# Performance work log

Measured on AMD Instinct MI355X. Metric: run time of the kernel, lower is better.

The kernel has to match this reference:

```python
import jax, jax.numpy as jnp
import numpy as np

BN_EPS = 1e-5


def setup_inputs() -> dict:
    key = jax.random.key(0)
    ks = jax.random.split(key, 10)
    B, C, Ci, H, W = 4, 256, 128, 64, 64
    s = 0.05
    return {
        "x": jax.random.normal(ks[0], (B, C, H, W), jnp.float32),
        "g_w": jax.random.normal(ks[1], (Ci, C), jnp.float32) * s,
        "g_b": jax.random.normal(ks[2], (Ci,), jnp.float32) * s,
        "theta_w": jax.random.normal(ks[3], (Ci, C), jnp.float32) * s,
        "theta_b": jax.random.normal(ks[4], (Ci,), jnp.float32) * s,
        "phi_w": jax.random.normal(ks[5], (Ci, C), jnp.float32) * s,
        "phi_b": jax.random.normal(ks[6], (Ci,), jnp.float32) * s,
        "W_w": jax.random.normal(ks[7], (C, Ci), jnp.float32) * s,
        "W_b": jax.random.normal(ks[8], (C,), jnp.float32) * s,
        "bn_gamma": jnp.ones((C,), jnp.float32),
        "bn_beta": jnp.zeros((C,), jnp.float32),
        "scale": jax.random.normal(ks[9], (1,), jnp.float32),
    }


def reference(x, g_w, g_b, theta_w, theta_b, phi_w, phi_b, W_w, W_b, bn_gamma, bn_beta, scale):
    B, C, H, W = x.shape
    xf = x.reshape(B, C, H * W)  # [B, C, N]
    # 1x1 conv projections == channel matmuls
    g = jnp.einsum('oc,bcn->bno', g_w, xf) + g_b            # [B, N, Ci]
    th = jnp.einsum('oc,bcn->bno', theta_w, xf) + theta_b   # [B, N, Ci]
    ph = jnp.einsum('oc,bcn->bon', phi_w, xf) + phi_b[:, None]  # [B, Ci, N]
    # unscaled attention: f = theta @ phi, softmax over keys
    f = jnp.einsum('bnd,bdm->bnm', th, ph)                  # [B, N, N]
    attn = jax.nn.softmax(f, axis=-1)
    y = jnp.einsum('bnm,bmo->bno', attn, g)                 # [B, N, Ci]
    y4 = y.transpose(0, 2, 1).reshape(B, -1, H, W)          # [B, Ci, H, W]
    # W: 1x1 conv + BatchNorm2d (training mode: batch statistics)
    wy = jnp.einsum('od,bdhw->bohw', W_w, y4) + W_b[None, :, None, None]
    mean = wy.mean(axis=(0, 2, 3))
    var = wy.var(axis=(0, 2, 3))
    bn = (wy - mean[None, :, None, None]) * jax.lax.rsqrt(var[None, :, None, None] + BN_EPS)
    bn = bn * bn_gamma[None, :, None, None] + bn_beta[None, :, None, None]
    return scale * bn + x
```

## Files before the change

kernel.cpp:

```cpp
#include <hip/hip_runtime.h>
#include <hip/hip_bf16.h>

#define BB 4
#define CC 256
#define CI 128
#define NN 4096

typedef _Float16 f16;
typedef __attribute__((ext_vector_type(8))) _Float16 f16x8;
typedef __attribute__((ext_vector_type(4))) _Float16 f16x4;
typedef __attribute__((ext_vector_type(4))) float f32x4;

#define MFMA(a,b,c) __builtin_amdgcn_mfma_f32_16x16x32_f16(a,b,c,0,0,0)
#define LDS3(p) ((__attribute__((address_space(3))) void*)(p))
#define GL1(p)  ((const __attribute__((address_space(1))) void*)(p))

__global__ __launch_bounds__(256) void k01_xpose(const float* x, f16* xt,
                                                 const float* tw, const float* pw,
                                                 const float* gw, const float* Ww, f16* wdst){
    int nt = blockIdx.x, ct = blockIdx.y, b = blockIdx.z;
    __shared__ float tile[64][65];
    int t = threadIdx.x;
    const float* src = x + ((size_t)(b*CC + ct*64))*NN + nt*64;
    #pragma unroll
    for (int k=0;k<16;k++){ int idx=t+k*256; int cl=idx>>6, nl=idx&63;
        tile[cl][nl]=src[(size_t)cl*NN + nl]; }
    __syncthreads();
    f16* dst = xt + ((size_t)(b*NN + nt*64))*CC + ct*64;
    #pragma unroll
    for (int k=0;k<16;k++){ int idx=t+k*256; int nl=idx>>6, cl=idx&63;
        dst[(size_t)nl*CC + cl] = (f16)tile[cl][nl]; }
    if (t < 128){
        int blkId = blockIdx.x + 64*(blockIdx.y + 4*blockIdx.z);
        int i = blkId*128 + t;
        int j = i & 32767; int sel = i >> 15;
        const float* s = (sel==0)? tw : (sel==1)? pw : (sel==2)? gw : Ww;
        wdst[i] = (f16)s[j];
    }
}

__global__ __launch_bounds__(256) void k2_all(const f16* xt, const f16* thw, const f16* phw,
                                              const f16* gwh, const float* thb, const float* phb,
                                              const float* gb, f16* th, f16* ph, f16* gt2){
    int b = blockIdx.y; int xx = blockIdx.x;
    int wv = threadIdx.x>>6, lane = threadIdx.x&63, q=lane>>4, cc=lane&15;
    if (xx < 64){
        int mat = xx>>5; int ntile = xx&31;
        int n0 = ntile*128 + wv*32;
        f16x8 aq[2][8];
        #pragma unroll
        for (int ns=0;ns<2;ns++){
            const f16* ap = xt + ((size_t)(b*NN + n0 + ns*16 + cc))*CC + q*8;
            #pragma unroll
            for (int kk=0;kk<8;kk++) aq[ns][kk] = *(const f16x8*)(ap + kk*32);
        }
        const f16* w   = mat? phw : thw;
        const float* bias = mat? phb : thb;
        f16* o = mat? ph : th;
        #pragma unroll 2
        for (int os=0;os<8;os++){
            f32x4 acc0={0,0,0,0}, acc1={0,0,0,0};
            const f16* wp = w + ((size_t)(os*16 + cc))*CC + q*8;
            #pragma unroll
            for (int kk=0;kk<8;kk++){
                f16x8 bf = *(const f16x8*)(wp + kk*32);
                acc0 = MFMA(aq[0][kk], bf, acc0);
                acc1 = MFMA(aq[1][kk], bf, acc1);
            }
            float bv = bias[os*16+cc];
            #pragma unroll
            for (int r=0;r<4;r++){
                o[((size_t)(b*NN + n0      + 4*q + r))*CI + os*16 + cc] = (f16)(acc0[r] + bv);
                o[((size_t)(b*NN + n0 + 16 + 4*q + r))*CI + os*16 + cc] = (f16)(acc1[r] + bv);
            }
        }
    } else {
        int mt = xx - 64;
        f16x8 ag[2][8];
        #pragma unroll
        for (int os=0;os<2;os++){
            const f16* ap = gwh + ((size_t)(wv*32 + os*16 + cc))*CC + q*8;
            #pragma unroll
            for (int kk=0;kk<8;kk++) ag[os][kk] = *(const f16x8*)(ap + kk*32);
        }
        f32x4 acc[2][4];
        #pragma unroll
        for (int os=0;os<2;os++){
            #pragma unroll
            for (int ms=0;ms<4;ms++) acc[os][ms]=(f32x4){0,0,0,0};
        }
        #pragma unroll 2
        for (int kk=0;kk<8;kk++){
            #pragma unroll
            for (int ms=0;ms<4;ms++){
                f16x8 bf = *(const f16x8*)(xt + ((size_t)(b*NN + mt*64 + ms*16 + cc))*CC + kk*32 + q*8);
                acc[0][ms]=MFMA(ag[0][kk],bf,acc[0][ms]);
                acc[1][ms]=MFMA(ag[1][kk],bf,acc[1][ms]);
            }
        }
        #pragma unroll
        for (int os=0;os<2;os++){
            #pragma unroll
            for (int r=0;r<4;r++){
                int orow = wv*32 + os*16 + 4*q + r;
                float bv = gb[orow];
                #pragma unroll
                for (int ms=0;ms<4;ms++){
                    int pos = (ms>>1)*32 + 8*(cc>>2) + 4*(ms&1) + (cc&3);
                    gt2[((size_t)(b*64 + mt))*8192 + orow*64 + pos] = (f16)(acc[os][ms][r] + bv);
                }
            }
        }
    }
}

__global__ __launch_bounds__(256, 2) void k3_attn(const f16* th, const f16* ph, const f16* gt2,
                                                  f16* ypart, float* ml){
    int qt = blockIdx.x;
    int sp = blockIdx.y;
    int b  = blockIdx.z;
    int wv=threadIdx.x>>6, lane=threadIdx.x&63, q=lane>>4, cc=lane&15;
    int qrow0 = qt*128 + wv*32;
    int kv0 = sp*1024;
    int sw  = cc<<4;
    int rsw = (cc&7)<<4;

    __shared__ __align__(16) char ldsb[65536];
    char* phL = ldsb;
    char* gtL = ldsb + 32768;

    f16x8 aq[2][4];
    #pragma unroll
    for (int rb=0;rb<2;rb++){
        const f16* thp = th + ((size_t)(b*NN + qrow0 + rb*16 + cc))*CI + q*8;
        #pragma unroll
        for (int kk=0;kk<4;kk++) aq[rb][kk] = *(const f16x8*)(thp + kk*32);
    }

    const char* phg = (const char*)(ph + (size_t)b*NN*CI);
    const char* gtg = (const char*)gt2 + (size_t)b*64*16384;

    f32x4 yacc[2][8];
    #pragma unroll
    for (int rb=0;rb<2;rb++)
        #pragma unroll
        for (int os=0;os<8;os++) yacc[rb][os]=(f32x4){0,0,0,0};
    float m_run0=-1e30f, m_run1=-1e30f, l_run0=0.f, l_run1=0.f;

    auto STAGE = [&](int tt, int bb){
        int key0 = kv0 + tt*64;
        int mt  = key0 >> 6;
        char* pbase = phL + bb*16384 + wv*4096;
        char* gbase = gtL + bb*16384 + wv*4096;
        #pragma unroll
        for (int ch=0; ch<4; ch++){
            int prow = wv*16 + ch*4 + (lane>>4);
            const char* ps = phg + (size_t)(key0 + prow)*256 + (((lane&15)*16) ^ ((prow&15)<<4));
            __builtin_amdgcn_global_load_lds(GL1(ps), LDS3(pbase + ch*1024), 16, 0, 0);
            int gf = wv*4096 + ch*1024 + lane*16;
            int grow = gf>>7, gcol = gf&127;
            int scol = gcol ^ ((grow&7)<<4);
            const char* gs = gtg + (size_t)mt*16384 + grow*128 + scol;
            __builtin_amdgcn_global_load_lds(GL1(gs), LDS3(gbase + ch*1024), 16, 0, 0);
        }
    };

    STAGE(0, 0);
    __syncthreads();

    int cur = 0;
    #pragma unroll 1
    for (int it=0; it<16; ++it){
        if (it < 15) STAGE(it+1, cur^1);
        const char* pt  = phL + cur*16384;
        const char* gtt = gtL + cur*16384;
        f32x4 fa[2][4];
        #pragma unroll
        for (int j=0;j<4;j++){
            f16x8 pf[4];
            #pragma unroll
            for (int kk=0;kk<4;kk++)
                pf[kk] = *(const f16x8*)(pt + (j*16+cc)*256 + ((kk*64 + q*16) ^ sw));
            fa[0][j]=(f32x4){0,0,0,0}; fa[1][j]=(f32x4){0,0,0,0};
            #pragma unroll
            for (int kk=0;kk<4;kk++){
                fa[0][j]=MFMA(pf[kk], aq[0][kk], fa[0][j]);
                fa[1][j]=MFMA(pf[kk], aq[1][kk], fa[1][j]);
            }
        }
        float pm0 = fmaxf(fmaxf(fmaxf(fa[0][0][0],fa[0][0][1]),fmaxf(fa[0][0][2],fa[0][0][3])),
                          fmaxf(fmaxf(fa[0][1][0],fa[0][1][1]),fmaxf(fa[0][1][2],fa[0][1][3])));
        pm0 = fmaxf(pm0, fmaxf(fmaxf(fa[0][2][0],fa[0][2][1]),fmaxf(fa[0][2][2],fa[0][2][3])));
        pm0 = fmaxf(pm0, fmaxf(fmaxf(fa[0][3][0],fa[0][3][1]),fmaxf(fa[0][3][2],fa[0][3][3])));
        float pm1 = fmaxf(fmaxf(fmaxf(fa[1][0][0],fa[1][0][1]),fmaxf(fa[1][0][2],fa[1][0][3])),
                          fmaxf(fmaxf(fa[1][1][0],fa[1][1][1]),fmaxf(fa[1][1][2],fa[1][1][3])));
        pm1 = fmaxf(pm1, fmaxf(fmaxf(fa[1][2][0],fa[1][2][1]),fmaxf(fa[1][2][2],fa[1][2][3])));
        pm1 = fmaxf(pm1, fmaxf(fmaxf(fa[1][3][0],fa[1][3][1]),fmaxf(fa[1][3][2],fa[1][3][3])));
        if (__any(fmaxf(pm0 - m_run0, pm1 - m_run1) > 3.f)){
            float mx0 = pm0;
            mx0 = fmaxf(mx0, __shfl_xor(mx0,16));
            mx0 = fmaxf(mx0, __shfl_xor(mx0,32));
            float mx1 = pm1;
            mx1 = fmaxf(mx1, __shfl_xor(mx1,16));
            mx1 = fmaxf(mx1, __shfl_xor(mx1,32));
            float nm0 = fmaxf(m_run0, mx0), nm1 = fmaxf(m_run1, mx1);
            float co0 = __expf(m_run0 - nm0), co1 = __expf(m_run1 - nm1);
            m_run0 = nm0; m_run1 = nm1;
            l_run0 *= co0; l_run1 *= co1;
            #pragma unroll
            for (int os=0;os<8;os++){ yacc[0][os] *= co0; yacc[1][os] *= co1; }
        }
        #pragma unroll
        for (int j=0;j<4;j++){
            #pragma unroll
            for (int r=0;r<4;r++){
                fa[0][j][r] = __expf(fa[0][j][r]-m_run0);
                fa[1][j][r] = __expf(fa[1][j][r]-m_run1);
            }
        }
        l_run0 += ((fa[0][0][0]+fa[0][0][1]+fa[0][0][2]+fa[0][0][3])
                 + (fa[0][1][0]+fa[0][1][1]+fa[0][1][2]+fa[0][1][3]))
                + ((fa[0][2][0]+fa[0][2][1]+fa[0][2][2]+fa[0][2][3])
                 + (fa[0][3][0]+fa[0][3][1]+fa[0][3][2]+fa[0][3][3]));
        l_run1 += ((fa[1][0][0]+fa[1][0][1]+fa[1][0][2]+fa[1][0][3])
                 + (fa[1][1][0]+fa[1][1][1]+fa[1][1][2]+fa[1][1][3]))
                + ((fa[1][2][0]+fa[1][2][1]+fa[1][2][2]+fa[1][2][3])
                 + (fa[1][3][0]+fa[1][3][1]+fa[1][3][2]+fa[1][3][3]));
        f16x8 pb0h0, pb0h1, pb1h0, pb1h1;
        #pragma unroll
        for (int r=0;r<4;r++){
            pb0h0[r]=(f16)fa[0][0][r]; pb0h0[4+r]=(f16)fa[0][1][r];
            pb0h1[r]=(f16)fa[0][2][r]; pb0h1[4+r]=(f16)fa[0][3][r];
            pb1h0[r]=(f16)fa[1][0][r]; pb1h0[4+r]=(f16)fa[1][1][r];
            pb1h1[r]=(f16)fa[1][2][r]; pb1h1[4+r]=(f16)fa[1][3][r];
        }
        #pragma unroll
        for (int os=0;os<8;os++){
            int row = os*16 + cc;
            f16x8 ga0 = *(const f16x8*)(gtt + row*128 + (((0<<6)|(q<<4)) ^ rsw));
            f16x8 ga1 = *(const f16x8*)(gtt + row*128 + (((1<<6)|(q<<4)) ^ rsw));
            yacc[0][os] = MFMA(ga0, pb0h0, yacc[0][os]);
            yacc[1][os] = MFMA(ga0, pb1h0, yacc[1][os]);
            yacc[0][os] = MFMA(ga1, pb0h1, yacc[0][os]);
            yacc[1][os] = MFMA(ga1, pb1h1, yacc[1][os]);
        }
        __syncthreads();
        cur ^= 1;
    }
    float l0 = l_run0; l0 += __shfl_xor(l0,16); l0 += __shfl_xor(l0,32);
    float l1 = l_run1; l1 += __shfl_xor(l1,16); l1 += __shfl_xor(l1,32);
    float linv0 = 1.f/l0, linv1 = 1.f/l1;
    f16* yl = (f16*)(ldsb + wv*8192);
    #pragma unroll
    for (int os=0;os<8;os++){
        #pragma unroll
        for (int r=0;r<4;r++){
            int o = os*16 + 4*q + r;
            *(f16*)((char*)yl + cc*256      + ((o*2) ^ ((cc&7)<<4))) = (f16)(yacc[0][os][r]*linv0);
            *(f16*)((char*)yl + (16+cc)*256 + ((o*2) ^ ((cc&7)<<4))) = (f16)(yacc[1][os][r]*linv1);
        }
    }
    #pragma unroll
    for (int p=0;p<8;p++){
        int idx = p*512 + lane*8;
        int row = idx>>7, o0 = idx&127;
        f16x8 v = *(const f16x8*)((char*)yl + row*256 + ((o0*2) ^ ((row&7)<<4)));
        *(f16x8*)(ypart + ((size_t)((sp*4+b)*NN + qrow0 + row))*CI + o0) = v;
    }
    if (lane < 16){
        size_t row0 = (size_t)(sp*4+b)*NN + qrow0 + lane;
        ml[row0*2]        = m_run0;
        ml[row0*2+1]      = l0;
        ml[(row0+16)*2]   = m_run1;
        ml[(row0+16)*2+1] = l1;
    }
}

__global__ __launch_bounds__(256) void k3c(const f16* ypart, const float* ml,
                                           f16* y, float* part, float* mupart){
    int blk = blockIdx.x; int t = threadIdx.x;
    int rloc = t>>2;
    int row  = blk*64 + rloc;
    int b = row>>12, n = row & 4095;
    int o0 = (t&3)*32;
    __shared__ __align__(16) f16 ldsT[128*64];
    float m_s[4], l_s[4];
    #pragma unroll
    for (int s=0;s<4;s++){ size_t r2 = ((size_t)(s*4+b)*NN + n)*2; m_s[s]=ml[r2]; l_s[s]=ml[r2+1]; }
    float M = fmaxf(fmaxf(m_s[0],m_s[1]),fmaxf(m_s[2],m_s[3]));
    float w[4]; float L=0.f;
    #pragma unroll
    for (int s=0;s<4;s++){ w[s]=l_s[s]*__expf(m_s[s]-M); L+=w[s]; }
    float inv = 1.f/L;
    #pragma unroll
    for (int s=0;s<4;s++) w[s]*=inv;
    float acc[32];
    #pragma unroll
    for (int j=0;j<32;j++) acc[j]=0.f;
    #pragma unroll
    for (int s=0;s<4;s++){
        const f16* src = ypart + ((size_t)(s*4+b)*NN + n)*CI + o0;
        #pragma unroll
        for (int v=0;v<4;v++){
            f16x8 vv = *(const f16x8*)(src + v*8);
            #pragma unroll
            for (int e=0;e<8;e++) acc[v*8+e] += w[s]*(float)vv[e];
        }
    }
    f16* yo = y + (size_t)row*CI + o0;
    #pragma unroll
    for (int v=0;v<4;v++){
        f16x8 ov;
        #pragma unroll
        for (int e=0;e<8;e++) ov[e] = (f16)acc[v*8+e];
        *(f16x8*)(yo + v*8) = ov;
        #pragma unroll
        for (int e=0;e<8;e++){
            int o = o0 + v*8 + e;
            ldsT[o*64 + (rloc ^ ((o&7)<<3))] = ov[e];
        }
    }
    __syncthreads();
    int wv=t>>6, lane=t&63, q=lane>>4, cc=lane&15;
    f32x4 gacc[2][8];
    #pragma unroll
    for (int a=0;a<2;a++)
        #pragma unroll
        for (int c2=0;c2<8;c2++) gacc[a][c2]=(f32x4){0,0,0,0};
    f16x8 af[2][2];
    #pragma unroll
    for (int o1t=0;o1t<2;o1t++){
        int o1 = (wv*2+o1t)*16+cc;
        #pragma unroll
        for (int kk=0;kk<2;kk++)
            af[o1t][kk] = *(const f16x8*)(ldsT + o1*64 + ((kk*32+q*8) ^ ((o1&7)<<3)));
    }
    #pragma unroll 1
    for (int o2t=0;o2t<8;o2t++){
        int o2 = o2t*16+cc;
        #pragma unroll
        for (int kk=0;kk<2;kk++){
            f16x8 bf = *(const f16x8*)(ldsT + o2*64 + ((kk*32+q*8) ^ ((o2&7)<<3)));
            gacc[0][o2t] = MFMA(af[0][kk], bf, gacc[0][o2t]);
            gacc[1][o2t] = MFMA(af[1][kk], bf, gacc[1][o2t]);
        }
    }
    float* pb = part + (size_t)blk*16384;
    #pragma unroll
    for (int o1t=0;o1t<2;o1t++){
        #pragma unroll
        for (int o2t=0;o2t<8;o2t++){
            #pragma unroll
            for (int r=0;r<4;r++)
                pb[((wv*2+o1t)*16+4*q+r)*128 + o2t*16+cc] = gacc[o1t][o2t][r];
        }
    }
    if (t<128){
        float sm=0.f;
        #pragma unroll
        for (int v=0;v<8;v++){
            f16x8 vv = *(const f16x8*)(ldsT + t*64 + ((v*8) ^ ((t&7)<<3)));
            #pragma unroll
            for (int e=0;e<8;e++) sm += (float)vv[e];
        }
        mupart[blk*128 + t] = sm;
    }
}

__global__ __launch_bounds__(256) void k4b_red(const float* part, const float* mupart, float* S){
    int pc = blockIdx.y;
    int t = threadIdx.x;
    if (blockIdx.x < 64){
        int i = blockIdx.x*256 + t;
        float s=0.f;
        #pragma unroll 1
        for (int p=pc*32; p<pc*32+32; p++) s += part[(size_t)p*16384 + i];
        atomicAdd(&S[i], s);
    } else if (t < 128){
        float s=0.f;
        #pragma unroll 1
        for (int p=pc*32; p<pc*32+32; p++) s += mupart[p*128 + t];
        atomicAdd(&S[16384+t], s);
    }
}

__global__ __launch_bounds__(128) void k4c_coef(const float* S, const float* Ww, const float* Wb,
                                                const float* gamma, const float* beta,
                                                const float* scale, float* AB){
    int ch = blockIdx.x; int t = threadIdx.x;
    const float* w = Ww + ch*CI;
    float tmp=0.f;
    const float* Srow = S + t*CI;
    #pragma unroll 1
    for (int o2=0;o2<CI;o2++) tmp += Srow[o2]*w[o2];
    float v  = w[t]*tmp;
    float mc = w[t]*S[16384 + t];
    #pragma unroll
    for (int s=1;s<64;s<<=1){ v += __shfl_xor(v,s); mc += __shfl_xor(mc,s); }
    __shared__ float red[4];
    if ((t&63)==0){ red[(t>>6)*2]=v; red[(t>>6)*2+1]=mc; }
    __syncthreads();
    if (t==0){
        float wSw = red[0]+red[2];
        float wmu = red[1]+red[3];
        const float M = 16384.f;
        float meanwy = wmu/M + Wb[ch];
        float var = wSw/M - (wmu/M)*(wmu/M);
        float inv = rsqrtf(var + 1e-5f);
        float sc = scale[0];
        float A  = sc*gamma[ch]*inv;
        float B3 = sc*(beta[ch] - meanwy*inv*gamma[ch]);
        AB[ch]     = A;
        AB[256+ch] = B3 + A*Wb[ch];
    }
}

__global__ __launch_bounds__(256) void k5_out(const f16* Wwh, const f16* y, const float* x,
                                              const float* AB, float* out){
    int ntile = blockIdx.x;
    int cht   = blockIdx.y;
    int b     = blockIdx.z;
    int wv=threadIdx.x>>6, lane=threadIdx.x&63, q=lane>>4, cc=lane&15;
    int ch0 = cht*64 + wv*16;
    f16x8 aw[4];
    const f16* wp = Wwh + ((size_t)(ch0+cc))*CI + q*8;
    #pragma unroll
    for (int kk=0;kk<4;kk++) aw[kk]=*(const f16x8*)(wp+kk*32);
    float Ar[4], Br[4];
    #pragma unroll
    for (int r=0;r<4;r++){ Ar[r]=AB[ch0+4*q+r]; Br[r]=AB[256+ch0+4*q+r]; }
    #pragma unroll 2
    for (int ns=0;ns<8;ns++){
        int n0 = ntile*128 + ns*16;
        f32x4 acc={0,0,0,0};
        const f16* yp = y + ((size_t)(b*NN + n0 + cc))*CI + q*8;
        #pragma unroll
        for (int kk=0;kk<4;kk++) acc = MFMA(aw[kk], *(const f16x8*)(yp+kk*32), acc);
        #pragma unroll
        for (int r=0;r<4;r++){
            size_t addr = ((size_t)(b*CC + ch0 + 4*q + r))*NN + n0 + cc;
            out[addr] = x[addr] + Ar[r]*acc[r] + Br[r];
        }
    }
}

extern "C" void kernel_launch(void* const* d_in, const int* in_sizes, int n_in,
                              void* d_out, int out_size, void* d_ws, size_t ws_size,
                              hipStream_t stream){
    const float* x    = (const float*)d_in[0];
    const float* g_w  = (const float*)d_in[1];
    const float* g_b  = (const float*)d_in[2];
    const float* th_w = (const float*)d_in[3];
    const float* th_b = (const float*)d_in[4];
    const float* ph_w = (const float*)d_in[5];
    const float* ph_b = (const float*)d_in[6];
    const float* W_w  = (const float*)d_in[7];
    const float* W_b  = (const float*)d_in[8];
    const float* bg   = (const float*)d_in[9];
    const float* bb   = (const float*)d_in[10];
    const float* sc   = (const float*)d_in[11];

    char* ws = (char*)d_ws;
    f16* xt  = (f16*)(ws);
    f16* th  = (f16*)(ws + 8388608);
    f16* ph  = (f16*)(ws + 8388608 + 1*4194304);
    f16* gt2 = (f16*)(ws + 8388608 + 2*4194304);
    f16* y   = (f16*)(ws + 8388608 + 3*4194304);
    f16* wh  = (f16*)(ws + 8388608 + 4*4194304);
    float* ml    = (float*)(ws + 25427968);
    f16*   ypart = (f16*)(ws + 25952256);
    float* mupart= (float*)(ws + 42729472);
    float* part  = (float*)ws;
    float* S    = (float*)(ws + 42860544);
    float* AB   = (float*)(ws + 42926592);
    f16* th_wh = wh;
    f16* ph_wh = wh + 32768;
    f16* g_wh  = wh + 65536;
    f16* Ww_h  = wh + 98304;

    hipMemsetAsync(S, 0, 16512*sizeof(float), stream);
    hipLaunchKernelGGL(k01_xpose, dim3(64,4,4), dim3(256), 0, stream, x, xt, th_w, ph_w, g_w, W_w, wh);
    hipLaunchKernelGGL(k2_all,   dim3(128,4),   dim3(256), 0, stream, xt, th_wh, ph_wh, g_wh,
                       th_b, ph_b, g_b, th, ph, gt2);
    hipLaunchKernelGGL(k3_attn,  dim3(32,4,4),  dim3(256), 0, stream, th, ph, gt2, ypart, ml);
    hipLaunchKernelGGL(k3c,      dim3(256),     dim3(256), 0, stream, ypart, ml, y, part, mupart);
    hipLaunchKernelGGL(k4b_red,  dim3(65,8),    dim3(256), 0, stream, part, mupart, S);
    hipLaunchKernelGGL(k4c_coef, dim3(256),     dim3(128), 0, stream, S, W_w, W_b, bg, bb, sc, AB);
    hipLaunchKernelGGL(k5_out,   dim3(32,4,4),  dim3(256), 0, stream, Ww_h, y, x, AB, (float*)d_out);
}
```

Before: 138.6 us.

## Add 8-way key-split attention kernel with single-buffered phi and smaller LDS

Adds k3_attn8, which splits the key dimension into 8 chunks of 512 instead of 4 of 1024, doubling the grid to 1024 blocks. It single-buffers the phi tile in LDS (48KB total) and targets 3 blocks per CU, to raise occupancy and parallelism on the attention stage. The combine kernel now loops over a runtime split count, which doubles the partial-output traffic it reads and writes. The 8-way path is only used when the workspace is at least about 60MB, so whether it runs depends on the harness allocation.

After: 149.0 us. +7.5%, slower.

```diff
diff --git a/kernel.cpp b/kernel.cpp
--- a/kernel.cpp
+++ b/kernel.cpp
@@ -116,9 +116,7 @@
 
 __global__ __launch_bounds__(256, 2) void k3_attn(const f16* th, const f16* ph, const f16* gt2,
                                                   f16* ypart, float* ml){
-    int qt = blockIdx.x;
-    int sp = blockIdx.y;
-    int b  = blockIdx.z;
+    int qt = blockIdx.x; int sp = blockIdx.y; int b = blockIdx.z;
     int wv=threadIdx.x>>6, lane=threadIdx.x&63, q=lane>>4, cc=lane&15;
     int qrow0 = qt*128 + wv*32;
     int kv0 = sp*1024;
@@ -136,7 +134,6 @@
         #pragma unroll
         for (int kk=0;kk<4;kk++) aq[rb][kk] = *(const f16x8*)(thp + kk*32);
     }
-
     const char* phg = (const char*)(ph + (size_t)b*NN*CI);
     const char* gtg = (const char*)gt2 + (size_t)b*64*16384;
 
@@ -167,7 +164,6 @@
 
     STAGE(0, 0);
     __syncthreads();
-
     int cur = 0;
     #pragma unroll 1
     for (int it=0; it<16; ++it){
@@ -276,35 +272,208 @@
     }
 }
 
+__global__ __launch_bounds__(256, 3) void k3_attn8(const f16* th, const f16* ph, const f16* gt2,
+                                                   f16* ypart, float* ml){
+    int qt = blockIdx.x;
+    int sp = blockIdx.y;
+    int b  = blockIdx.z;
+    int wv=threadIdx.x>>6, lane=threadIdx.x&63, q=lane>>4, cc=lane&15;
+    int qrow0 = qt*128 + wv*32;
+    int kv0 = sp*512;
+    int sw  = cc<<4;
+    int rsw = (cc&7)<<4;
+
+    __shared__ __align__(16) char ldsb[49152];
+    char* phL = ldsb;
+    char* gtL = ldsb + 16384;
+
+    f16x8 aq[2][4];
+    #pragma unroll
+    for (int rb=0;rb<2;rb++){
+        const f16* thp = th + ((size_t)(b*NN + qrow0 + rb*16 + cc))*CI + q*8;
+        #pragma unroll
+        for (int kk=0;kk<4;kk++) aq[rb][kk] = *(const f16x8*)(thp + kk*32);
+    }
+    const char* phg = (const char*)(ph + (size_t)b*NN*CI);
+    const char* gtg = (const char*)gt2 + (size_t)b*64*16384;
+
+    f32x4 yacc[2][8];
+    #pragma unroll
+    for (int rb=0;rb<2;rb++)
+        #pragma unroll
+        for (int os=0;os<8;os++) yacc[rb][os]=(f32x4){0,0,0,0};
+    float m_run0=-1e30f, m_run1=-1e30f, l_run0=0.f, l_run1=0.f;
+
+    auto STAGE_PH = [&](int tt){
+        int key0 = kv0 + tt*64;
+        char* pbase = phL + wv*4096;
+        #pragma unroll
+        for (int ch=0; ch<4; ch++){
+            int prow = wv*16 + ch*4 + (lane>>4);
+            const char* ps = phg + (size_t)(key0 + prow)*256 + (((lane&15)*16) ^ ((prow&15)<<4));
+            __builtin_amdgcn_global_load_lds(GL1(ps), LDS3(pbase + ch*1024), 16, 0, 0);
+        }
+    };
+    auto STAGE_GT = [&](int tt, int bb){
+        int key0 = kv0 + tt*64;
+        int mt  = key0 >> 6;
+        char* gbase = gtL + bb*16384 + wv*4096;
+        #pragma unroll
+        for (int ch=0; ch<4; ch++){
+            int gf = wv*4096 + ch*1024 + lane*16;
+            int grow = gf>>7, gcol = gf&127;
+            int scol = gcol ^ ((grow&7)<<4);
+            const char* gs = gtg + (size_t)mt*16384 + grow*128 + scol;
+            __builtin_amdgcn_global_load_lds(GL1(gs), LDS3(gbase + ch*1024), 16, 0, 0);
+        }
+    };
+
+    STAGE_PH(0);
+    STAGE_GT(0, 0);
+    __syncthreads();
+
+    int cur = 0;
+    #pragma unroll 1
+    for (int it=0; it<8; ++it){
+        f32x4 fa[2][4];
+        #pragma unroll
+        for (int j=0;j<4;j++){
+            f16x8 pf[4];
+            #pragma unroll
+            for (int kk=0;kk<4;kk++)
+                pf[kk] = *(const f16x8*)(phL + (j*16+cc)*256 + ((kk*64 + q*16) ^ sw));
+            fa[0][j]=(f32x4){0,0,0,0}; fa[1][j]=(f32x4){0,0,0,0};
+            #pragma unroll
+            for (int kk=0;kk<4;kk++){
+                fa[0][j]=MFMA(pf[kk], aq[0][kk], fa[0][j]);
+                fa[1][j]=MFMA(pf[kk], aq[1][kk], fa[1][j]);
+            }
+        }
+        __syncthreads();
+        if (it < 7){
+            STAGE_PH(it+1);
+            STAGE_GT(it+1, cur^1);
+        }
+        float pm0 = fmaxf(fmaxf(fmaxf(fa[0][0][0],fa[0][0][1]),fmaxf(fa[0][0][2],fa[0][0][3])),
+                          fmaxf(fmaxf(fa[0][1][0],fa[0][1][1]),fmaxf(fa[0][1][2],fa[0][1][3])));
+        pm0 = fmaxf(pm0, fmaxf(fmaxf(fa[0][2][0],fa[0][2][1]),fmaxf(fa[0][2][2],fa[0][2][3])));
+        pm0 = fmaxf(pm0, fmaxf(fmaxf(fa[0][3][0],fa[0][3][1]),fmaxf(fa[0][3][2],fa[0][3][3])));
+        float pm1 = fmaxf(fmaxf(fmaxf(fa[1][0][0],fa[1][0][1]),fmaxf(fa[1][0][2],fa[1][0][3])),
+                          fmaxf(fmaxf(fa[1][1][0],fa[1][1][1]),fmaxf(fa[1][1][2],fa[1][1][3])));
+        pm1 = fmaxf(pm1, fmaxf(fmaxf(fa[1][2][0],fa[1][2][1]),fmaxf(fa[1][2][2],fa[1][2][3])));
+        pm1 = fmaxf(pm1, fmaxf(fmaxf(fa[1][3][0],fa[1][3][1]),fmaxf(fa[1][3][2],fa[1][3][3])));
+        if (__any(fmaxf(pm0 - m_run0, pm1 - m_run1) > 3.f)){
+            float mx0 = pm0;
+            mx0 = fmaxf(mx0, __shfl_xor(mx0,16));
+            mx0 = fmaxf(mx0, __shfl_xor(mx0,32));
+            float mx1 = pm1;
+            mx1 = fmaxf(mx1, __shfl_xor(mx1,16));
+            mx1 = fmaxf(mx1, __shfl_xor(mx1,32));
+            float nm0 = fmaxf(m_run0, mx0), nm1 = fmaxf(m_run1, mx1);
+            float co0 = __expf(m_run0 - nm0), co1 = __expf(m_run1 - nm1);
+            m_run0 = nm0; m_run1 = nm1;
+            l_run0 *= co0; l_run1 *= co1;
+            #pragma unroll
+            for (int os=0;os<8;os++){ yacc[0][os] *= co0; yacc[1][os] *= co1; }
+        }
+        #pragma unroll
+        for (int j=0;j<4;j++){
+            #pragma unroll
+            for (int r=0;r<4;r++){
+                fa[0][j][r] = __expf(fa[0][j][r]-m_run0);
+                fa[1][j][r] = __expf(fa[1][j][r]-m_run1);
+            }
+        }
+        l_run0 += ((fa[0][0][0]+fa[0][0][1]+fa[0][0][2]+fa[0][0][3])
+                 + (fa[0][1][0]+fa[0][1][1]+fa[0][1][2]+fa[0][1][3]))
+                + ((fa[0][2][0]+fa[0][2][1]+fa[0][2][2]+fa[0][2][3])
+                 + (fa[0][3][0]+fa[0][3][1]+fa[0][3][2]+fa[0][3][3]));
+        l_run1 += ((fa[1][0][0]+fa[1][0][1]+fa[1][0][2]+fa[1][0][3])
+                 + (fa[1][1][0]+fa[1][1][1]+fa[1][1][2]+fa[1][1][3]))
+                + ((fa[1][2][0]+fa[1][2][1]+fa[1][2][2]+fa[1][2][3])
+                 + (fa[1][3][0]+fa[1][3][1]+fa[1][3][2]+fa[1][3][3]));
+        f16x8 pb0h0, pb0h1, pb1h0, pb1h1;
+        #pragma unroll
+        for (int r=0;r<4;r++){
+            pb0h0[r]=(f16)fa[0][0][r]; pb0h0[4+r]=(f16)fa[0][1][r];
+            pb0h1[r]=(f16)fa[0][2][r]; pb0h1[4+r]=(f16)fa[0][3][r];
+            pb1h0[r]=(f16)fa[1][0][r]; pb1h0[4+r]=(f16)fa[1][1][r];
+            pb1h1[r]=(f16)fa[1][2][r]; pb1h1[4+r]=(f16)fa[1][3][r];
+        }
+        const char* gtt = gtL + cur*16384;
+        #pragma unroll
+        for (int os=0;os<8;os++){
+            int row = os*16 + cc;
+            f16x8 ga0 = *(const f16x8*)(gtt + row*128 + (((0<<6)|(q<<4)) ^ rsw));
+            f16x8 ga1 = *(const f16x8*)(gtt + row*128 + (((1<<6)|(q<<4)) ^ rsw));
+            yacc[0][os] = MFMA(ga0, pb0h0, yacc[0][os]);
+            yacc[1][os] = MFMA(ga0, pb1h0, yacc[1][os]);
+            yacc[0][os] = MFMA(ga1, pb0h1, yacc[0][os]);
+            yacc[1][os] = MFMA(ga1, pb1h1, yacc[1][os]);
+        }
+        __syncthreads();
+        cur ^= 1;
+    }
+    float l0 = l_run0; l0 += __shfl_xor(l0,16); l0 += __shfl_xor(l0,32);
+    float l1 = l_run1; l1 += __shfl_xor(l1,16); l1 += __shfl_xor(l1,32);
+    float linv0 = 1.f/l0, linv1 = 1.f/l1;
+    f16* yl = (f16*)(ldsb + wv*8192);
+    #pragma unroll
+    for (int os=0;os<8;os++){
+        #pragma unroll
+        for (int r=0;r<4;r++){
+            int o = os*16 + 4*q + r;
+            *(f16*)((char*)yl + cc*256      + ((o*2) ^ ((cc&7)<<4))) = (f16)(yacc[0][os][r]*linv0);
+            *(f16*)((char*)yl + (16+cc)*256 + ((o*2) ^ ((cc&7)<<4))) = (f16)(yacc[1][os][r]*linv1);
+        }
+    }
+    #pragma unroll
+    for (int p=0;p<8;p++){
+        int idx = p*512 + lane*8;
+        int row = idx>>7, o0 = idx&127;
+        f16x8 v = *(const f16x8*)((char*)yl + row*256 + ((o0*2) ^ ((row&7)<<4)));
+        *(f16x8*)(ypart + ((size_t)((sp*4+b)*NN + qrow0 + row))*CI + o0) = v;
+    }
+    if (lane < 16){
+        size_t row0 = (size_t)(sp*4+b)*NN + qrow0 + lane;
+        ml[row0*2]        = m_run0;
+        ml[row0*2+1]      = l0;
+        ml[(row0+16)*2]   = m_run1;
+        ml[(row0+16)*2+1] = l1;
+    }
+}
+
 __global__ __launch_bounds__(256) void k3c(const f16* ypart, const float* ml,
-                                           f16* y, float* part, float* mupart){
+                                           f16* y, float* part, float* mupart, int nsp){
     int blk = blockIdx.x; int t = threadIdx.x;
     int rloc = t>>2;
     int row  = blk*64 + rloc;
     int b = row>>12, n = row & 4095;
     int o0 = (t&3)*32;
     __shared__ __align__(16) f16 ldsT[128*64];
-    float m_s[4], l_s[4];
-    #pragma unroll
-    for (int s=0;s<4;s++){ size_t r2 = ((size_t)(s*4+b)*NN + n)*2; m_s[s]=ml[r2]; l_s[s]=ml[r2+1]; }
-    float M = fmaxf(fmaxf(m_s[0],m_s[1]),fmaxf(m_s[2],m_s[3]));
-    float w[4]; float L=0.f;
-    #pragma unroll
-    for (int s=0;s<4;s++){ w[s]=l_s[s]*__expf(m_s[s]-M); L+=w[s]; }
+    float M = -1e30f;
+    #pragma unroll 1
+    for (int s=0;s<nsp;s++) M = fmaxf(M, ml[((size_t)(s*4+b)*NN + n)*2]);
+    float L = 0.f;
+    #pragma unroll 1
+    for (int s=0;s<nsp;s++){
+        size_t r2 = ((size_t)(s*4+b)*NN + n)*2;
+        L += ml[r2+1]*__expf(ml[r2]-M);
+    }
     float inv = 1.f/L;
-    #pragma unroll
-    for (int s=0;s<4;s++) w[s]*=inv;
     float acc[32];
     #pragma unroll
     for (int j=0;j<32;j++) acc[j]=0.f;
-    #pragma unroll
-    for (int s=0;s<4;s++){
+    #pragma unroll 1
+    for (int s=0;s<nsp;s++){
+        size_t r2 = ((size_t)(s*4+b)*NN + n)*2;
+        float w = ml[r2+1]*__expf(ml[r2]-M)*inv;
         const f16* src = ypart + ((size_t)(s*4+b)*NN + n)*CI + o0;
         #pragma unroll
         for (int v=0;v<4;v++){
             f16x8 vv = *(const f16x8*)(src + v*8);
             #pragma unroll
-            for (int e=0;e<8;e++) acc[v*8+e] += w[s]*(float)vv[e];
+            for (int e=0;e<8;e++) acc[v*8+e] += w*(float)vv[e];
         }
     }
     f16* yo = y + (size_t)row*CI + o0;
@@ -461,18 +630,38 @@
     const float* sc   = (const float*)d_in[11];
 
     char* ws = (char*)d_ws;
-    f16* xt  = (f16*)(ws);
-    f16* th  = (f16*)(ws + 8388608);
-    f16* ph  = (f16*)(ws + 8388608 + 1*4194304);
-    f16* gt2 = (f16*)(ws + 8388608 + 2*4194304);
-    f16* y   = (f16*)(ws + 8388608 + 3*4194304);
-    f16* wh  = (f16*)(ws + 8388608 + 4*4194304);
-    float* ml    = (float*)(ws + 25427968);
-    f16*   ypart = (f16*)(ws + 25952256);
-    float* mupart= (float*)(ws + 42729472);
-    float* part  = (float*)ws;
-    float* S    = (float*)(ws + 42860544);
-    float* AB   = (float*)(ws + 42926592);
+    const size_t NEED8 = 60300000ull;
+    int nsp = (ws_size >= NEED8) ? 8 : 4;
+
+    f16 *xt, *th, *ph, *gt2, *y, *wh, *ypart;
+    float *ml, *part, *mupart, *S, *AB;
+    if (nsp == 8){
+        xt    = (f16*)(ws);
+        th    = (f16*)(ws + 8388608);
+        ph    = (f16*)(ws + 12582912);
+        gt2   = (f16*)(ws + 16777216);
+        wh    = (f16*)(ws + 20971520);
+        ml    = (float*)(ws + 21233664);
+        y     = (f16*)(ws + 22282240);
+        ypart = (f16*)(ws + 26476544);
+        S     = (float*)(ws + 60030976);
+        AB    = (float*)(ws + 60097024);
+        mupart= (float*)(ws + 60099072);
+        part  = (float*)ws;
+    } else {
+        xt    = (f16*)(ws);
+        th    = (f16*)(ws + 8388608);
+        ph    = (f16*)(ws + 12582912);
+        gt2   = (f16*)(ws + 16777216);
+        y     = (f16*)(ws + 20971520);
+        wh    = (f16*)(ws + 25165824);
+        ml    = (float*)(ws + 25427968);
+        ypart = (f16*)(ws + 25952256);
+        mupart= (float*)(ws + 42729472);
+        part  = (float*)ws;
+        S     = (float*)(ws + 42860544);
+        AB    = (float*)(ws + 42926592);
+    }
     f16* th_wh = wh;
     f16* ph_wh = wh + 32768;
     f16* g_wh  = wh + 65536;
@@ -482,8 +671,11 @@
     hipLaunchKernelGGL(k01_xpose, dim3(64,4,4), dim3(256), 0, stream, x, xt, th_w, ph_w, g_w, W_w, wh);
     hipLaunchKernelGGL(k2_all,   dim3(128,4),   dim3(256), 0, stream, xt, th_wh, ph_wh, g_wh,
                        th_b, ph_b, g_b, th, ph, gt2);
-    hipLaunchKernelGGL(k3_attn,  dim3(32,4,4),  dim3(256), 0, stream, th, ph, gt2, ypart, ml);
-    hipLaunchKernelGGL(k3c,      dim3(256),     dim3(256), 0, stream, ypart, ml, y, part, mupart);
+    if (nsp == 8)
+        hipLaunchKernelGGL(k3_attn8, dim3(32,8,4), dim3(256), 0, stream, th, ph, gt2, ypart, ml);
+    else
+        hipLaunchKernelGGL(k3_attn,  dim3(32,4,4), dim3(256), 0, stream, th, ph, gt2, ypart, ml);
+    hipLaunchKernelGGL(k3c,      dim3(256),     dim3(256), 0, stream, ypart, ml, y, part, mupart, nsp);
     hipLaunchKernelGGL(k4b_red,  dim3(65,8),    dim3(256), 0, stream, part, mupart, S);
     hipLaunchKernelGGL(k4c_coef, dim3(256),     dim3(128), 0, stream, S, W_w, W_b, bg, bb, sc, AB);
     hipLaunchKernelGGL(k5_out,   dim3(32,4,4),  dim3(256), 0, stream, Ww_h, y, x, AB, (float*)d_out);
```
